# Optimization experiments

Hardware: AMD Instinct MI355X
Metric: run time of the kernel (lower is better)

Reference implementation:

```python
import jax, jax.numpy as jnp
import numpy as np
import math

T = 120      # frame_num == audio_len == max_seq_len
D = 64       # hidden_layer_size
H = 2        # n_head
DH = D // H
DFF = 2 * D
DOUT = 31
PERIOD = 10
EPS = 1e-5
NEG = -1e9
SCALE = 1.0 / math.sqrt(DH)
SLOPES = (1.0 / 16.0, 1.0 / 256.0)  # ALiBi slopes for n_head=2


def _pe():
    # PeriodicPositionalEncoding: sinusoid over one period, tiled
    pos = jnp.arange(PERIOD, dtype=jnp.float32)[:, None]
    div = jnp.exp(jnp.arange(0, D, 2, dtype=jnp.float32) * (-math.log(10000.0) / D))
    s, c = jnp.sin(pos * div), jnp.cos(pos * div)
    pe = jnp.stack([s, c], axis=-1).reshape(PERIOD, D)  # interleave sin/cos
    return jnp.tile(pe, (T // PERIOD + 1, 1))[:T]


def _alibi_mask():
    # causal mask + ALiBi bias: alibi[i,j] = -slope * floor((i-j)/period) for j<=i
    slopes = jnp.array(SLOPES, dtype=jnp.float32)
    i = jnp.arange(T)[:, None]
    j = jnp.arange(T)[None, :]
    rel = ((i - j) // PERIOD).astype(jnp.float32)
    return jnp.where(j <= i, -slopes[:, None, None] * rel, NEG)  # [H,T,T]


def _ln(x, g, b):
    m = x.mean(-1, keepdims=True)
    v = ((x - m) ** 2).mean(-1, keepdims=True)
    return (x - m) / jnp.sqrt(v + EPS) * g + b


def setup_inputs() -> dict:
    key = jax.random.key(0)
    ks = iter(jax.random.split(key, 32))
    n = lambda shape, s=0.05: jax.random.normal(next(ks), shape, dtype=jnp.float32) * s
    inp = {
        'audio': jax.random.normal(next(ks), (1, T, 1024), dtype=jnp.float32),
        'W_audio': n((D, 1024)), 'b_audio': n((D,)),
        'obj_W': n((D, 5)),
        'Wq': n((D, D)), 'bq': n((D,)), 'Wk': n((D, D)), 'bk': n((D,)),
        'Wv': n((D, D)), 'bv': n((D,)), 'Wo': n((D, D)), 'bo': n((D,)),
        'Wv2': n((D, D)), 'bv2': n((D,)), 'Wo2': n((D, D)), 'bo2': n((D,)),
        'g1': jnp.ones((D,)), 'be1': jnp.zeros((D,)),
        'g2': jnp.ones((D,)), 'be2': jnp.zeros((D,)),
        'g3': jnp.ones((D,)), 'be3': jnp.zeros((D,)),
        'W1': n((DFF, D)), 'c1': n((DFF,)), 'W2': n((D, DFF)), 'c2': n((D,)),
        'Wr': n((DOUT, D)), 'br': n((DOUT,)), 'Wm': n((D, DOUT)), 'bm': n((D,)),
    }
    return inp


def _forward(audio, W_audio, b_audio, obj_W, Wq, bq, Wk, bk, Wv, bv, Wo, bo,
             Wv2, bv2, Wo2, bo2, g1, be1, g2, be2, g3, be3,
             W1, c1, W2, c2, Wr, br, Wm, bm):
    mem = audio[0] @ W_audio.T + b_audio          # [S,D], S == T
    style = obj_W[:, 0]                            # obj_vector @ [1,0,0,0,0]
    pe = _pe()
    mask = _alibi_mask()
    slopes = jnp.array(SLOPES, dtype=jnp.float32)
    jarr = jnp.arange(T)

    # enc_dec_mask leaves exactly one memory key per target row (anti-diagonal
    # from the end); the feedback row t at step t always attends memory[-1],
    # so its cross-attn output is just the projected value of the last frame.
    cross_last = (mem[-1] @ Wv2.T + bv2) @ Wo2.T + bo2  # [D]

    def step(emb, t):
        # decode only the last row (row t) of the growing sequence; 1-layer
        # post-norm decoder => row t depends only on input rows 0..t.
        x = emb + pe                                 # PPE over prefix
        xq = jnp.take(x, t, axis=0)                  # [D]
        q = (xq @ Wq.T + bq).reshape(H, DH)
        k = (x @ Wk.T + bk).reshape(T, H, DH)
        v = (x @ Wv.T + bv).reshape(T, H, DH)
        bias = jnp.where(jarr <= t,
                         -slopes[:, None] * ((t - jarr) // PERIOD).astype(jnp.float32),
                         NEG)                        # [H,T]
        sc = jnp.einsum('hd,shd->hs', q, k) * SCALE + bias
        a = jax.nn.softmax(sc, axis=-1)
        sa = jnp.einsum('hs,shd->hd', a, v).reshape(D) @ Wo.T + bo
        h1 = _ln(xq + sa, g1, be1)
        h2 = _ln(h1 + cross_last, g2, be2)
        h3 = _ln(h2 + jax.nn.relu(h2 @ W1.T + c1) @ W2.T + c2, g3, be3)
        new = (h3 @ Wr.T + br) @ Wm.T + bm + style   # vertice_map(vertice_map_r(.)) + style
        emb = jax.lax.dynamic_update_slice(emb, new[None, :], (t + 1, 0))
        return emb, None

    emb0 = jnp.zeros((T, D), audio.dtype).at[0].set(style)
    emb, _ = jax.lax.scan(step, emb0, jnp.arange(T - 1))

    # final full-length decode (last loop iteration of the torch module)
    x = emb + pe
    q = (x @ Wq.T + bq).reshape(T, H, DH)
    k = (x @ Wk.T + bk).reshape(T, H, DH)
    v = (x @ Wv.T + bv).reshape(T, H, DH)
    sc = jnp.einsum('thd,shd->hts', q, k) * SCALE + mask
    a = jax.nn.softmax(sc, axis=-1)
    sa = jnp.einsum('hts,shd->thd', a, v).reshape(T, D) @ Wo.T + bo
    h1 = _ln(x + sa, g1, be1)
    # at length T with S == T the enc_dec_mask aligns target row j <-> memory row j
    cross = (mem @ Wv2.T + bv2) @ Wo2.T + bo2
    h2 = _ln(h1 + cross, g2, be2)
    h3 = _ln(h2 + jax.nn.relu(h2 @ W1.T + c1) @ W2.T + c2, g3, be3)
    return (h3 @ Wr.T + br)[None]                    # [1,T,31]


def reference(audio, W_audio, b_audio, obj_W, Wq, bq, Wk, bk, Wv, bv, Wo, bo,
              Wv2, bv2, Wo2, bo2, g1, be1, g2, be2, g3, be3,
              W1, c1, W2, c2, Wr, br, Wm, bm):
    return _forward(audio, W_audio, b_audio, obj_W, Wq, bq, Wk, bk, Wv, bv, Wo, bo,
                    Wv2, bv2, Wo2, bo2, g1, be1, g2, be2, g3, be3,
                    W1, c1, W2, c2, Wr, br, Wm, bm)
```

## Files before the change

kernel.cpp:

```cpp
#include <hip/hip_runtime.h>

typedef unsigned short u16;
typedef unsigned int   u32;
typedef _Float16 f16;
typedef f16 h2 __attribute__((ext_vector_type(2)));
typedef f16 h4 __attribute__((ext_vector_type(4)));
typedef f16 h8 __attribute__((ext_vector_type(8)));

#define T_    120
#define D_    64
#define DFF_  128
#define DOUT_ 31
#define KROW_ 68
#define VROW_ 132

#if defined(__has_builtin)
#if __has_builtin(__builtin_amdgcn_fdot2)
#define DOT2(a,b,c) __builtin_amdgcn_fdot2((a),(b),(c),false)
#endif
#endif
#ifndef DOT2
#define DOT2(a,b,c) ((float)(a).x*(float)(b).x + ((float)(a).y*(float)(b).y + (c)))
#endif
#define SHV(x,i,j) __builtin_shufflevector((x),(x),(i),(j))

__device__ __forceinline__ h2 pk(float a, float b){
#if defined(__has_builtin) && __has_builtin(__builtin_amdgcn_cvt_pkrtz)
  return __builtin_bit_cast(h2, __builtin_amdgcn_cvt_pkrtz(a, b));
#else
  h2 r; r.x = (f16)a; r.y = (f16)b; return r;
#endif
}

__device__ __forceinline__ float b2f(u16 u){ return __uint_as_float(((u32)u) << 16); }
__device__ __forceinline__ float2 bp2(u32 u){
  float2 r; r.x = __uint_as_float(u << 16); r.y = __uint_as_float(u & 0xffff0000u); return r;
}
__device__ __forceinline__ u16 f2bu(float f){
  u32 u = __float_as_uint(f);
  u32 r = u + 0x7fffu + ((u >> 16) & 1u);
  return (u16)(r >> 16);
}
#define WSYNC() do{ __asm__ __volatile__("" ::: "memory"); __builtin_amdgcn_wave_barrier(); }while(0)

__device__ __forceinline__ float dpp_sum(float x){
  int t;
  t = __builtin_amdgcn_update_dpp(0, __float_as_int(x), 0x111, 0xf, 0xf, true); x += __int_as_float(t);
  t = __builtin_amdgcn_update_dpp(0, __float_as_int(x), 0x112, 0xf, 0xf, true); x += __int_as_float(t);
  t = __builtin_amdgcn_update_dpp(0, __float_as_int(x), 0x114, 0xf, 0xf, true); x += __int_as_float(t);
  t = __builtin_amdgcn_update_dpp(0, __float_as_int(x), 0x118, 0xf, 0xf, true); x += __int_as_float(t);
  t = __builtin_amdgcn_update_dpp(0, __float_as_int(x), 0x142, 0xf, 0xf, true); x += __int_as_float(t);
  t = __builtin_amdgcn_update_dpp(0, __float_as_int(x), 0x143, 0xf, 0xf, true); x += __int_as_float(t);
  return __int_as_float(__builtin_amdgcn_readlane(__float_as_int(x), 63));
}
__device__ __forceinline__ float dpp_max_pos(float x){
  int t;
  t = __builtin_amdgcn_update_dpp(0, __float_as_int(x), 0x111, 0xf, 0xf, true); x = fmaxf(x, __int_as_float(t));
  t = __builtin_amdgcn_update_dpp(0, __float_as_int(x), 0x112, 0xf, 0xf, true); x = fmaxf(x, __int_as_float(t));
  t = __builtin_amdgcn_update_dpp(0, __float_as_int(x), 0x114, 0xf, 0xf, true); x = fmaxf(x, __int_as_float(t));
  t = __builtin_amdgcn_update_dpp(0, __float_as_int(x), 0x118, 0xf, 0xf, true); x = fmaxf(x, __int_as_float(t));
  t = __builtin_amdgcn_update_dpp(0, __float_as_int(x), 0x142, 0xf, 0xf, true); x = fmaxf(x, __int_as_float(t));
  t = __builtin_amdgcn_update_dpp(0, __float_as_int(x), 0x143, 0xf, 0xf, true); x = fmaxf(x, __int_as_float(t));
  return __int_as_float(__builtin_amdgcn_readlane(__float_as_int(x), 63));
}
__device__ __forceinline__ float pe_val(int row, int i){
  const float coef = -0.28782313662425574f;
  int p = row % 10;
  float dv  = __expf((float)(i >> 1) * coef);
  float ang = (float)p * dv;
  return (i & 1) ? __cosf(ang) : __sinf(ang);
}
__device__ __forceinline__ void loadrow32(h2* dst, const float* row){
  #pragma unroll
  for (int r = 0; r < 16; ++r){
    float4 f = ((const float4*)row)[r];
    dst[2*r]   = pk(f.x, f.y);
    dst[2*r+1] = pk(f.z, f.w);
  }
}
__device__ __forceinline__ void loadrow64(h2* dst, const float* row){
  #pragma unroll
  for (int r = 0; r < 32; ++r){
    float4 f = ((const float4*)row)[r];
    dst[2*r]   = pk(f.x, f.y);
    dst[2*r+1] = pk(f.z, f.w);
  }
}

__global__ __launch_bounds__(256) void k_prep(const float* __restrict__ Wv, const float* __restrict__ Wo,
                                              const float* __restrict__ W1, const float* __restrict__ W2,
                                              const float* __restrict__ Wr,
                                              u16* __restrict__ wvb, u16* __restrict__ wob,
                                              u16* __restrict__ w1b, u16* __restrict__ w2b,
                                              u16* __restrict__ wrb){
  int i0 = blockIdx.x*256 + threadIdx.x, stride = gridDim.x*256;
  for (int i = i0; i < 4096; i += stride){ wvb[i] = f2bu(Wv[i]); wob[i] = f2bu(Wo[i]); }
  for (int i = i0; i < 8192; i += stride){ w1b[i] = f2bu(W1[i]); w2b[i] = f2bu(W2[i]); }
  for (int i = i0; i < 1984; i += stride){ wrb[i] = f2bu(Wr[i]); }
}

__global__ __launch_bounds__(256) void k_mem(const float* __restrict__ audio,
                                             const float* __restrict__ Wa,
                                             const float* __restrict__ ba,
                                             float* __restrict__ mem){
  __shared__ float ash[1024];
  const int t = blockIdx.x, tid = threadIdx.x;
  for (int i = tid; i < 1024; i += 256) ash[i] = audio[t*1024 + i];
  __syncthreads();
  const int w = tid >> 6, lane = tid & 63;
  for (int d = w*16; d < w*16 + 16; ++d){
    const float4* row = (const float4*)(Wa + d*1024);
    float acc = 0.f;
    #pragma unroll
    for (int m = 0; m < 4; ++m){
      float4 wp = row[lane + 64*m];
      int j = 4*(lane + 64*m);
      acc += wp.x*ash[j] + wp.y*ash[j+1] + wp.z*ash[j+2] + wp.w*ash[j+3];
    }
    acc = dpp_sum(acc);
    if (lane == 0) mem[t*64 + d] = acc + ba[d];
  }
}

__global__ __launch_bounds__(64) void k_cross(const float* __restrict__ mem,
                                              const float* __restrict__ Wv2, const float* __restrict__ bv2,
                                              const float* __restrict__ Wo2, const float* __restrict__ bo2,
                                              float* __restrict__ cross){
  __shared__ float msh[64], tsh[64];
  const int t = blockIdx.x, i = threadIdx.x;
  msh[i] = mem[t*64 + i];
  __syncthreads();
  const float4* r1 = (const float4*)(Wv2 + i*64);
  float a = bv2[i];
  #pragma unroll
  for (int j = 0; j < 16; ++j){ float4 w = r1[j]; a += w.x*msh[4*j] + w.y*msh[4*j+1] + w.z*msh[4*j+2] + w.w*msh[4*j+3]; }
  tsh[i] = a;
  __syncthreads();
  const float4* r2 = (const float4*)(Wo2 + i*64);
  float c = bo2[i];
  #pragma unroll
  for (int j = 0; j < 16; ++j){ float4 w = r2[j]; c += w.x*tsh[4*j] + w.y*tsh[4*j+1] + w.z*tsh[4*j+2] + w.w*tsh[4*j+3]; }
  cross[t*64 + i] = c;
}

__global__ __launch_bounds__(128, 1) void k_scan(
    const float* __restrict__ objW,
    const float* __restrict__ Wq, const float* __restrict__ bq,
    const float* __restrict__ Wk, const float* __restrict__ bk,
    const float* __restrict__ Wv, const float* __restrict__ bv,
    const float* __restrict__ Wo, const float* __restrict__ bo,
    const float* __restrict__ g1, const float* __restrict__ be1,
    const float* __restrict__ g2, const float* __restrict__ be2,
    const float* __restrict__ g3, const float* __restrict__ be3,
    const float* __restrict__ W1, const float* __restrict__ c1,
    const float* __restrict__ W2, const float* __restrict__ c2,
    const float* __restrict__ Wr, const float* __restrict__ br,
    const float* __restrict__ Wm, const float* __restrict__ bm,
    const float* __restrict__ cross,
    float* __restrict__ xw, float* __restrict__ Kw, float* __restrict__ Vw)
{
  __shared__ __align__(16) f16 KcS[128*KROW_];
  __shared__ __align__(16) f16 VcS[D_*VROW_];
  __shared__ __align__(16) f16 sch[256];
  __shared__ __align__(16) f16 xh[64], qh[64], ath[64], h2h[64], h3h[64], rsh[32];
  __shared__ __align__(16) f16 fsh[128];
  __shared__ float at_p[64];
  __shared__ float pe_tab[640];

  const int tid = threadIdx.x;
  const int i = tid & 63;
  const bool w0 = tid < 64;

  h2 WA[32];
  h2 WB[32];
  h2 WOr[32], W1r[32], WRr[32], WMr[16];
  h2 W2r[64];
  float biasA=0.f, biasB=0.f, bo_r=0.f, c1r=0.f, c2_r=0.f, br_r=0.f, bmst=0.f, cls_r=0.f;
  float g1r=0.f,b1r=0.f,g2r=0.f,b2r=0.f,g3r=0.f,b3r=0.f, xr=0.f;

  if (w0){
    loadrow32(WA,  Wq + i*64);
    loadrow32(WB,  Wv + i*64);
    loadrow32(WOr, Wo + i*64);
    loadrow32(W1r, W1 + i*64);
    loadrow64(W2r, W2 + i*128);
    loadrow32(WRr, Wr + (i < 31 ? i : 30)*64);
    { const float* row = Wm + i*31;
      #pragma unroll
      for (int r = 0; r < 15; ++r) WMr[r] = pk(row[2*r], row[2*r+1]);
      WMr[15] = pk(row[30], 0.f); }
    biasA = bq[i]; biasB = bv[i]; bo_r = bo[i]; c1r = c1[i]; c2_r = c2[i];
    br_r = (i < 31) ? br[i] : 0.f;
    float st = objW[i*5];
    bmst = bm[i] + st;
    cls_r = cross[119*64 + i];
    g1r=g1[i]; b1r=be1[i]; g2r=g2[i]; b2r=be2[i]; g3r=g3[i]; b3r=be3[i];
    xr = st + pe_val(0, i);
    xh[i] = (f16)xr;
    xw[i] = xr;
  } else {
    loadrow32(WA, Wk + i*64);
    loadrow32(WB, W1 + (64+i)*64);
    biasA = bk[i]; c1r = c1[64+i];
  }
  { u32* kcw = (u32*)KcS; for (int idx = tid; idx < 128*KROW_/2; idx += 128) kcw[idx] = 0; }
  { u32* vcw = (u32*)VcS; for (int idx = tid; idx < D_*VROW_/2;  idx += 128) vcw[idx] = 0; }
  for (int idx = tid; idx < 640; idx += 128) pe_tab[idx] = pe_val(idx >> 6, idx & 63);
  if (tid < 32) rsh[tid] = (f16)0.f;
  __syncthreads();

  int pp = 1;
  for (int t = 0; t < T_-1; ++t){
    float atp0 = 0.f;
    {
      const h8* xv = (const h8*)xh;
      float a0=biasA, a1=0.f, a2=0.f, a3=0.f;
      #pragma unroll
      for (int r = 0; r < 8; ++r){
        h8 x = xv[r];
        a0 = DOT2(WA[4*r+0], SHV(x,0,1), a0);
        a1 = DOT2(WA[4*r+1], SHV(x,2,3), a1);
        a2 = DOT2(WA[4*r+2], SHV(x,4,5), a2);
        a3 = DOT2(WA[4*r+3], SHV(x,6,7), a3);
      }
      float accA = (a0+a1)+(a2+a3);
      if (w0){
        float b0=biasB, b1=0.f, b2=0.f, b3=0.f;
        #pragma unroll
        for (int r = 0; r < 8; ++r){
          h8 x = xv[r];
          b0 = DOT2(WB[4*r+0], SHV(x,0,1), b0);
          b1 = DOT2(WB[4*r+1], SHV(x,2,3), b1);
          b2 = DOT2(WB[4*r+2], SHV(x,4,5), b2);
          b3 = DOT2(WB[4*r+3], SHV(x,6,7), b3);
        }
        float accB = (b0+b1)+(b2+b3);
        qh[i] = (f16)accA;
        VcS[i*VROW_ + t] = (f16)accB;
        Vw[t*64 + i] = accB;
      } else {
        KcS[t*KROW_ + i] = (f16)accA;
        Kw[t*64 + i] = accA;
      }
    }
    __syncthreads();
    {
      const int h = tid >> 6, j = i;
      const h8* qv = (const h8*)(qh + h*32);
      const h4* k0 = (const h4*)(KcS + j*KROW_ + h*32);
      const h4* k1 = (const h4*)(KcS + (j+64)*KROW_ + h*32);
      float d0a=0.f,d0b=0.f,d1a=0.f,d1b=0.f;
      #pragma unroll
      for (int r = 0; r < 4; ++r){
        h8 q = qv[r];
        h4 ka = k0[2*r], kb = k0[2*r+1], kc = k1[2*r], kd = k1[2*r+1];
        d0a = DOT2(SHV(ka,0,1), SHV(q,0,1), d0a);
        d0b = DOT2(SHV(ka,2,3), SHV(q,2,3), d0b);
        d0a = DOT2(SHV(kb,0,1), SHV(q,4,5), d0a);
        d0b = DOT2(SHV(kb,2,3), SHV(q,6,7), d0b);
        d1a = DOT2(SHV(kc,0,1), SHV(q,0,1), d1a);
        d1b = DOT2(SHV(kc,2,3), SHV(q,2,3), d1b);
        d1a = DOT2(SHV(kd,0,1), SHV(q,4,5), d1a);
        d1b = DOT2(SHV(kd,2,3), SHV(q,6,7), d1b);
      }
      float d0 = d0a + d0b, d1 = d1a + d1b;
      const float slope = h ? 0.00390625f : 0.0625f;
      int r0 = (t - j) / 10, r1 = (t - j - 64) / 10;
      float s0 = (j      <= t) ? d0*0.17677669529663687f - slope*(float)r0 : -1e30f;
      float s1 = (j + 64 <= t) ? d1*0.17677669529663687f - slope*(float)r1 : -1e30f;
      float m = dpp_max_pos(fmaxf(s0, s1) + 16384.f) - 16384.f;
      float e0 = (j      <= t) ? __expf(s0 - m) : 0.f;
      float e1 = (j + 64 <= t) ? __expf(s1 - m) : 0.f;
      float inv = 1.f / dpp_sum(e0 + e1);
      sch[h*128 + j]      = (f16)(e0*inv);
      sch[h*128 + j + 64] = (f16)(e1*inv);
    }
    __syncthreads();
    {
      const int hd = i >> 5;
      const h8* av = (const h8*)(sch + hd*128) + (w0 ? 0 : 8);
      const h4* vv = (const h4*)(VcS + i*VROW_) + (w0 ? 0 : 16);
      float p0=0.f,p1=0.f,p2=0.f,p3=0.f;
      #pragma unroll
      for (int r = 0; r < 8; ++r){
        h8 a = av[r];
        h4 va = vv[2*r], vb = vv[2*r+1];
        p0 = DOT2(SHV(va,0,1), SHV(a,0,1), p0);
        p1 = DOT2(SHV(va,2,3), SHV(a,2,3), p1);
        p2 = DOT2(SHV(vb,0,1), SHV(a,4,5), p2);
        p3 = DOT2(SHV(vb,2,3), SHV(a,6,7), p3);
      }
      float p = (p0+p1)+(p2+p3);
      if (!w0) at_p[i] = p; else atp0 = p;
    }
    __syncthreads();
    if (w0){
      float atv = atp0 + at_p[i];
      ath[i] = (f16)atv;
      WSYNC();
      const h8* av = (const h8*)ath;
      float a0=bo_r, a1=0.f, a2=0.f, a3=0.f;
      #pragma unroll
      for (int r = 0; r < 8; ++r){
        h8 x = av[r];
        a0 = DOT2(WOr[4*r+0], SHV(x,0,1), a0);
        a1 = DOT2(WOr[4*r+1], SHV(x,2,3), a1);
        a2 = DOT2(WOr[4*r+2], SHV(x,4,5), a2);
        a3 = DOT2(WOr[4*r+3], SHV(x,6,7), a3);
      }
      float y = xr + (a0+a1)+(a2+a3);
      float s = dpp_sum(y), s2 = dpp_sum(y*y);
      float m = s*(1.f/64.f), var = fmaxf(s2*(1.f/64.f) - m*m, 0.f);
      float h1 = (y - m)*rsqrtf(var + 1e-5f)*g1r + b1r;
      float z = h1 + cls_r;
      float sz = dpp_sum(z), sz2 = dpp_sum(z*z);
      float mz = sz*(1.f/64.f), vz = fmaxf(sz2*(1.f/64.f) - mz*mz, 0.f);
      float h2v = (z - mz)*rsqrtf(vz + 1e-5f)*g2r + b2r;
      h2h[i] = (f16)h2v;
      at_p[i] = h2v;
    }
    __syncthreads();
    {
      const h8* hv = (const h8*)h2h;
      float a0=c1r, a1=0.f, a2=0.f, a3=0.f;
      if (w0){
        #pragma unroll
        for (int r = 0; r < 8; ++r){
          h8 x = hv[r];
          a0 = DOT2(W1r[4*r+0], SHV(x,0,1), a0);
          a1 = DOT2(W1r[4*r+1], SHV(x,2,3), a1);
          a2 = DOT2(W1r[4*r+2], SHV(x,4,5), a2);
          a3 = DOT2(W1r[4*r+3], SHV(x,6,7), a3);
        }
      } else {
        #pragma unroll
        for (int r = 0; r < 8; ++r){
          h8 x = hv[r];
          a0 = DOT2(WB[4*r+0], SHV(x,0,1), a0);
          a1 = DOT2(WB[4*r+1], SHV(x,2,3), a1);
          a2 = DOT2(WB[4*r+2], SHV(x,4,5), a2);
          a3 = DOT2(WB[4*r+3], SHV(x,6,7), a3);
        }
      }
      fsh[tid] = (f16)fmaxf((a0+a1)+(a2+a3), 0.f);
    }
    __syncthreads();
    if (w0){
      const h8* fv = (const h8*)fsh;
      float a0=c2_r, a1=0.f, a2=0.f, a3=0.f;
      #pragma unroll
      for (int r = 0; r < 16; ++r){
        h8 x = fv[r];
        a0 = DOT2(W2r[4*r+0], SHV(x,0,1), a0);
        a1 = DOT2(W2r[4*r+1], SHV(x,2,3), a1);
        a2 = DOT2(W2r[4*r+2], SHV(x,4,5), a2);
        a3 = DOT2(W2r[4*r+3], SHV(x,6,7), a3);
      }
      float y = at_p[i] + (a0+a1)+(a2+a3);
      float s = dpp_sum(y), s2 = dpp_sum(y*y);
      float m = s*(1.f/64.f), var = fmaxf(s2*(1.f/64.f) - m*m, 0.f);
      float h3v = (y - m)*rsqrtf(var + 1e-5f)*g3r + b3r;
      h3h[i] = (f16)h3v;
      WSYNC();
      const h8* h3v8 = (const h8*)h3h;
      float r0=br_r, r1=0.f, r2=0.f, r3=0.f;
      #pragma unroll
      for (int r = 0; r < 8; ++r){
        h8 x = h3v8[r];
        r0 = DOT2(WRr[4*r+0], SHV(x,0,1), r0);
        r1 = DOT2(WRr[4*r+1], SHV(x,2,3), r1);
        r2 = DOT2(WRr[4*r+2], SHV(x,4,5), r2);
        r3 = DOT2(WRr[4*r+3], SHV(x,6,7), r3);
      }
      if (i < 31) rsh[i] = (f16)((r0+r1)+(r2+r3));
      WSYNC();
      const h8* rv = (const h8*)rsh;
      float m0=bmst, m1=0.f, m2=0.f, m3=0.f;
      #pragma unroll
      for (int r = 0; r < 4; ++r){
        h8 x = rv[r];
        m0 = DOT2(WMr[4*r+0], SHV(x,0,1), m0);
        m1 = DOT2(WMr[4*r+1], SHV(x,2,3), m1);
        m2 = DOT2(WMr[4*r+2], SHV(x,4,5), m2);
        m3 = DOT2(WMr[4*r+3], SHV(x,6,7), m3);
      }
      float xn = (m0+m1)+(m2+m3) + pe_tab[pp*64 + i];
      xr = xn;
      xh[i] = (f16)xn;
      xw[(t+1)*64 + i] = xn;
    }
    __syncthreads();
    pp = (pp == 9) ? 0 : pp + 1;
  }
  {
    const h8* xv = (const h8*)xh;
    if (w0){
      float b0=biasB, b1=0.f, b2=0.f, b3=0.f;
      #pragma unroll
      for (int r = 0; r < 8; ++r){
        h8 x = xv[r];
        b0 = DOT2(WB[4*r+0], SHV(x,0,1), b0);
        b1 = DOT2(WB[4*r+1], SHV(x,2,3), b1);
        b2 = DOT2(WB[4*r+2], SHV(x,4,5), b2);
        b3 = DOT2(WB[4*r+3], SHV(x,6,7), b3);
      }
      Vw[119*64 + i] = (b0+b1)+(b2+b3);
    } else {
      float a0=biasA, a1=0.f, a2=0.f, a3=0.f;
      #pragma unroll
      for (int r = 0; r < 8; ++r){
        h8 x = xv[r];
        a0 = DOT2(WA[4*r+0], SHV(x,0,1), a0);
        a1 = DOT2(WA[4*r+1], SHV(x,2,3), a1);
        a2 = DOT2(WA[4*r+2], SHV(x,4,5), a2);
        a3 = DOT2(WA[4*r+3], SHV(x,6,7), a3);
      }
      Kw[119*64 + i] = (a0+a1)+(a2+a3);
    }
  }
}

__global__ __launch_bounds__(128) void k_final(
    const float* __restrict__ Wq, const float* __restrict__ bq, const float* __restrict__ bo,
    const float* __restrict__ g1, const float* __restrict__ be1,
    const float* __restrict__ g2, const float* __restrict__ be2,
    const float* __restrict__ g3, const float* __restrict__ be3,
    const float* __restrict__ c1, const float* __restrict__ c2, const float* __restrict__ br,
    const u16* __restrict__ wo_b, const u16* __restrict__ w1_b,
    const u16* __restrict__ w2_b, const u16* __restrict__ wr_b,
    const float* __restrict__ cross, const float* __restrict__ xw,
    const float* __restrict__ Kw, const float* __restrict__ Vw,
    float* __restrict__ out)
{
  __shared__ float xs[64], qs[64], at[64], h2s[64], h3s[64], fs[128], sc[256];
  const int irow = blockIdx.x, tid = threadIdx.x;
  if (tid < 64) xs[tid] = xw[irow*64 + tid];
  __syncthreads();
  if (tid < 64){
    const float4* wr_ = (const float4*)(Wq + tid*64);
    float acc = bq[tid];
    #pragma unroll
    for (int j = 0; j < 16; ++j){ float4 w = wr_[j]; acc += w.x*xs[4*j] + w.y*xs[4*j+1] + w.z*xs[4*j+2] + w.w*xs[4*j+3]; }
    qs[tid] = acc;
  }
  __syncthreads();
  {
    const int h = tid >> 6, j = tid & 63;
    const float* qh_ = qs + h*32;
    float d0 = 0.f, d1 = 0.f;
    const float4* k0 = (const float4*)(Kw + j*64 + h*32);
    #pragma unroll
    for (int w = 0; w < 8; ++w){ float4 p = k0[w]; d0 += p.x*qh_[4*w] + p.y*qh_[4*w+1] + p.z*qh_[4*w+2] + p.w*qh_[4*w+3]; }
    if (j < 56){
      const float4* k1 = (const float4*)(Kw + (j+64)*64 + h*32);
      #pragma unroll
      for (int w = 0; w < 8; ++w){ float4 p = k1[w]; d1 += p.x*qh_[4*w] + p.y*qh_[4*w+1] + p.z*qh_[4*w+2] + p.w*qh_[4*w+3]; }
    }
    const float slope = h ? 0.00390625f : 0.0625f;
    float s0 = (j      <= irow) ? d0*0.17677669529663687f - slope*(float)((irow-j)/10)    : -1e30f;
    float s1 = (j + 64 <= irow) ? d1*0.17677669529663687f - slope*(float)((irow-j-64)/10) : -1e30f;
    float m = dpp_max_pos(fmaxf(s0, s1) + 16384.f) - 16384.f;
    float e0 = (j      <= irow) ? __expf(s0 - m) : 0.f;
    float e1 = (j + 64 <= irow) ? __expf(s1 - m) : 0.f;
    float inv = 1.f / dpp_sum(e0 + e1);
    sc[h*128 + j]      = e0*inv;
    sc[h*128 + j + 64] = e1*inv;
  }
  __syncthreads();
  if (tid < 64){
    const float* a = sc + (tid >> 5)*128;
    float a0=0.f,a1=0.f,a2=0.f,a3=0.f;
    #pragma unroll
    for (int jj = 0; jj < 30; ++jj){
      a0 += a[4*jj]   * Vw[(4*jj)*64   + tid];
      a1 += a[4*jj+1] * Vw[(4*jj+1)*64 + tid];
      a2 += a[4*jj+2] * Vw[(4*jj+2)*64 + tid];
      a3 += a[4*jj+3] * Vw[(4*jj+3)*64 + tid];
    }
    at[tid] = (a0+a1)+(a2+a3);
  }
  __syncthreads();
  if (tid < 64){
    const u32* orow = (const u32*)(wo_b + tid*64);
    float acc = bo[tid];
    #pragma unroll
    for (int w = 0; w < 32; ++w){ float2 p = bp2(orow[w]); acc += p.x*at[2*w] + p.y*at[2*w+1]; }
    float y = xs[tid] + acc;
    float s = dpp_sum(y), s2 = dpp_sum(y*y);
    float m = s*(1.f/64.f), var = fmaxf(s2*(1.f/64.f) - m*m, 0.f);
    float h1 = (y - m)*rsqrtf(var + 1e-5f)*g1[tid] + be1[tid];
    float z = h1 + cross[irow*64 + tid];
    float sz = dpp_sum(z), sz2 = dpp_sum(z*z);
    float mz = sz*(1.f/64.f), vz = fmaxf(sz2*(1.f/64.f) - mz*mz, 0.f);
    h2s[tid] = (z - mz)*rsqrtf(vz + 1e-5f)*g2[tid] + be2[tid];
  }
  __syncthreads();
  {
    const u32* w1r = (const u32*)(w1_b + tid*64);
    float acc = c1[tid];
    #pragma unroll
    for (int w = 0; w < 32; ++w){ float2 p = bp2(w1r[w]); acc += p.x*h2s[2*w] + p.y*h2s[2*w+1]; }
    fs[tid] = fmaxf(acc, 0.f);
  }
  __syncthreads();
  if (tid < 64){
    const u32* w2r = (const u32*)(w2_b + tid*128);
    float acc = c2[tid];
    #pragma unroll
    for (int w = 0; w < 64; ++w){ float2 p = bp2(w2r[w]); acc += p.x*fs[2*w] + p.y*fs[2*w+1]; }
    float y = h2s[tid] + acc;
    float s = dpp_sum(y), s2 = dpp_sum(y*y);
    float m = s*(1.f/64.f), var = fmaxf(s2*(1.f/64.f) - m*m, 0.f);
    h3s[tid] = (y - m)*rsqrtf(var + 1e-5f)*g3[tid] + be3[tid];
  }
  __syncthreads();
  if (tid < DOUT_){
    const u32* rr = (const u32*)(wr_b + tid*64);
    float acc = br[tid];
    #pragma unroll
    for (int w = 0; w < 32; ++w){ float2 p = bp2(rr[w]); acc += p.x*h3s[2*w] + p.y*h3s[2*w+1]; }
    out[irow*DOUT_ + tid] = acc;
  }
}

extern "C" void kernel_launch(void* const* d_in, const int* in_sizes, int n_in,
                              void* d_out, int out_size, void* d_ws, size_t ws_size,
                              hipStream_t stream){
  const float* audio=(const float*)d_in[0];
  const float* Wa   =(const float*)d_in[1];
  const float* ba   =(const float*)d_in[2];
  const float* objW =(const float*)d_in[3];
  const float* Wq   =(const float*)d_in[4];
  const float* bq   =(const float*)d_in[5];
  const float* Wk   =(const float*)d_in[6];
  const float* bk   =(const float*)d_in[7];
  const float* Wv   =(const float*)d_in[8];
  const float* bv   =(const float*)d_in[9];
  const float* Wo   =(const float*)d_in[10];
  const float* bo   =(const float*)d_in[11];
  const float* Wv2  =(const float*)d_in[12];
  const float* bv2  =(const float*)d_in[13];
  const float* Wo2  =(const float*)d_in[14];
  const float* bo2  =(const float*)d_in[15];
  const float* g1   =(const float*)d_in[16];
  const float* be1  =(const float*)d_in[17];
  const float* g2   =(const float*)d_in[18];
  const float* be2  =(const float*)d_in[19];
  const float* g3   =(const float*)d_in[20];
  const float* be3  =(const float*)d_in[21];
  const float* W1   =(const float*)d_in[22];
  const float* c1   =(const float*)d_in[23];
  const float* W2   =(const float*)d_in[24];
  const float* c2   =(const float*)d_in[25];
  const float* Wr   =(const float*)d_in[26];
  const float* br   =(const float*)d_in[27];
  const float* Wm   =(const float*)d_in[28];
  const float* bm   =(const float*)d_in[29];

  float* ws    = (float*)d_ws;
  float* mem   = ws;
  float* cross = ws + 7680;
  float* xw    = ws + 15360;
  float* Kw    = ws + 23040;
  float* Vw    = ws + 30720;
  u16* bb   = (u16*)(ws + 38400);
  u16* wv_b = bb;
  u16* wo_b = bb + 4096;
  u16* w1_b = bb + 8192;
  u16* w2_b = bb + 16384;
  u16* wr_b = bb + 24576;
  float* out = (float*)d_out;

  k_prep <<<dim3(32),  dim3(256), 0, stream>>>(Wv, Wo, W1, W2, Wr, wv_b, wo_b, w1_b, w2_b, wr_b);
  k_mem  <<<dim3(120), dim3(256), 0, stream>>>(audio, Wa, ba, mem);
  k_cross<<<dim3(120), dim3(64),  0, stream>>>(mem, Wv2, bv2, Wo2, bo2, cross);
  k_scan <<<dim3(1),   dim3(128), 0, stream>>>(objW, Wq, bq, Wk, bk, Wv, bv, Wo, bo,
                                               g1, be1, g2, be2, g3, be3,
                                               W1, c1, W2, c2, Wr, br, Wm, bm,
                                               cross, xw, Kw, Vw);
  k_final<<<dim3(120), dim3(128), 0, stream>>>(Wq, bq, bo, g1, be1, g2, be2, g3, be3,
                                               c1, c2, br, wo_b, w1_b, w2_b, wr_b,
                                               cross, xw, Kw, Vw, out);
}
```

Before: 440.6 us.

## Fold Wm·Wr into one matrix, rebalance scan work across waves, fuse prep kernels

Precomputes Ms = Wm·Wr and bMv = Wm·br + bm, so the sequential scan step does one 64x64 matvec instead of two chained ones (64→31→64). The FFN second layer and the output/feedback path move to the second wave, which spreads register-held weights evenly across both waves and shortens the first wave's critical path. It also merges the prep, memory and cross kernels into one launch. K, V and x are kept in shared memory and written once as fp16 at the end, instead of fp32 global stores every step. The fused product and the fp16 storage change rounding slightly compared with the reference.

```diff
diff --git a/kernel.cpp b/kernel.cpp
--- a/kernel.cpp
+++ b/kernel.cpp
@@ -9,7 +9,6 @@
 
 #define T_    120
 #define D_    64
-#define DFF_  128
 #define DOUT_ 31
 #define KROW_ 68
 #define VROW_ 132
@@ -31,7 +30,6 @@
   h2 r; r.x = (f16)a; r.y = (f16)b; return r;
 #endif
 }
-
 __device__ __forceinline__ float b2f(u16 u){ return __uint_as_float(((u32)u) << 16); }
 __device__ __forceinline__ float2 bp2(u32 u){
   float2 r; r.x = __uint_as_float(u << 16); r.y = __uint_as_float(u & 0xffff0000u); return r;
@@ -40,6 +38,9 @@
   u32 u = __float_as_uint(f);
   u32 r = u + 0x7fffu + ((u >> 16) & 1u);
   return (u16)(r >> 16);
+}
+__device__ __forceinline__ u16 f2h16(float x){
+  f16 v = (f16)x; u16 r; __builtin_memcpy(&r, &v, 2); return r;
 }
 #define WSYNC() do{ __asm__ __volatile__("" ::: "memory"); __builtin_amdgcn_wave_barrier(); }while(0)
 
@@ -78,34 +79,42 @@
     dst[2*r+1] = pk(f.z, f.w);
   }
 }
-__device__ __forceinline__ void loadrow64(h2* dst, const float* row){
-  #pragma unroll
-  for (int r = 0; r < 32; ++r){
-    float4 f = ((const float4*)row)[r];
-    dst[2*r]   = pk(f.x, f.y);
-    dst[2*r+1] = pk(f.z, f.w);
-  }
-}
-
-__global__ __launch_bounds__(256) void k_prep(const float* __restrict__ Wv, const float* __restrict__ Wo,
-                                              const float* __restrict__ W1, const float* __restrict__ W2,
-                                              const float* __restrict__ Wr,
-                                              u16* __restrict__ wvb, u16* __restrict__ wob,
-                                              u16* __restrict__ w1b, u16* __restrict__ w2b,
-                                              u16* __restrict__ wrb){
-  int i0 = blockIdx.x*256 + threadIdx.x, stride = gridDim.x*256;
-  for (int i = i0; i < 4096; i += stride){ wvb[i] = f2bu(Wv[i]); wob[i] = f2bu(Wo[i]); }
-  for (int i = i0; i < 8192; i += stride){ w1b[i] = f2bu(W1[i]); w2b[i] = f2bu(W2[i]); }
-  for (int i = i0; i < 1984; i += stride){ wrb[i] = f2bu(Wr[i]); }
-}
-
-__global__ __launch_bounds__(256) void k_mem(const float* __restrict__ audio,
-                                             const float* __restrict__ Wa,
-                                             const float* __restrict__ ba,
-                                             float* __restrict__ mem){
+
+__global__ __launch_bounds__(256) void k_pre(const float* __restrict__ audio,
+                                             const float* __restrict__ Wa, const float* __restrict__ ba,
+                                             const float* __restrict__ Wv2, const float* __restrict__ bv2,
+                                             const float* __restrict__ Wo2, const float* __restrict__ bo2,
+                                             const float* __restrict__ Wo, const float* __restrict__ W1,
+                                             const float* __restrict__ W2, const float* __restrict__ Wr,
+                                             const float* __restrict__ Wm, const float* __restrict__ br,
+                                             const float* __restrict__ bm,
+                                             float* __restrict__ cross, float* __restrict__ Ms,
+                                             float* __restrict__ bMv,
+                                             u16* __restrict__ wob, u16* __restrict__ w1b,
+                                             u16* __restrict__ w2b, u16* __restrict__ wrb){
+  const int b = blockIdx.x, tid = threadIdx.x;
+  if (b == 120){
+    for (int i = tid; i < 4096; i += 256) wob[i] = f2bu(Wo[i]);
+    for (int i = tid; i < 8192; i += 256){ w1b[i] = f2bu(W1[i]); w2b[i] = f2bu(W2[i]); }
+    for (int i = tid; i < 1984; i += 256) wrb[i] = f2bu(Wr[i]);
+    for (int idx = tid; idx < 4096; idx += 256){
+      int d = idx >> 6, e = idx & 63;
+      float acc = 0.f;
+      #pragma unroll
+      for (int j = 0; j < 31; ++j) acc += Wm[d*31 + j] * Wr[j*64 + e];
+      Ms[idx] = acc;
+    }
+    if (tid < 64){
+      float acc = bm[tid];
+      #pragma unroll
+      for (int j = 0; j < 31; ++j) acc += Wm[tid*31 + j] * br[j];
+      bMv[tid] = acc;
+    }
+    return;
+  }
   __shared__ float ash[1024];
-  const int t = blockIdx.x, tid = threadIdx.x;
-  for (int i = tid; i < 1024; i += 256) ash[i] = audio[t*1024 + i];
+  __shared__ float msh[64], tsh[64];
+  for (int i = tid; i < 1024; i += 256) ash[i] = audio[b*1024 + i];
   __syncthreads();
   const int w = tid >> 6, lane = tid & 63;
   for (int d = w*16; d < w*16 + 16; ++d){
@@ -118,29 +127,24 @@
       acc += wp.x*ash[j] + wp.y*ash[j+1] + wp.z*ash[j+2] + wp.w*ash[j+3];
     }
     acc = dpp_sum(acc);
-    if (lane == 0) mem[t*64 + d] = acc + ba[d];
-  }
-}
-
-__global__ __launch_bounds__(64) void k_cross(const float* __restrict__ mem,
-                                              const float* __restrict__ Wv2, const float* __restrict__ bv2,
-                                              const float* __restrict__ Wo2, const float* __restrict__ bo2,
-                                              float* __restrict__ cross){
-  __shared__ float msh[64], tsh[64];
-  const int t = blockIdx.x, i = threadIdx.x;
-  msh[i] = mem[t*64 + i];
-  __syncthreads();
-  const float4* r1 = (const float4*)(Wv2 + i*64);
-  float a = bv2[i];
-  #pragma unroll
-  for (int j = 0; j < 16; ++j){ float4 w = r1[j]; a += w.x*msh[4*j] + w.y*msh[4*j+1] + w.z*msh[4*j+2] + w.w*msh[4*j+3]; }
-  tsh[i] = a;
-  __syncthreads();
-  const float4* r2 = (const float4*)(Wo2 + i*64);
-  float c = bo2[i];
-  #pragma unroll
-  for (int j = 0; j < 16; ++j){ float4 w = r2[j]; c += w.x*tsh[4*j] + w.y*tsh[4*j+1] + w.z*tsh[4*j+2] + w.w*tsh[4*j+3]; }
-  cross[t*64 + i] = c;
+    if (lane == 0) msh[d] = acc + ba[d];
+  }
+  __syncthreads();
+  if (tid < 64){
+    const float4* r1 = (const float4*)(Wv2 + tid*64);
+    float a = bv2[tid];
+    #pragma unroll
+    for (int j = 0; j < 16; ++j){ float4 p = r1[j]; a += p.x*msh[4*j] + p.y*msh[4*j+1] + p.z*msh[4*j+2] + p.w*msh[4*j+3]; }
+    tsh[tid] = a;
+  }
+  __syncthreads();
+  if (tid < 64){
+    const float4* r2 = (const float4*)(Wo2 + tid*64);
+    float c = bo2[tid];
+    #pragma unroll
+    for (int j = 0; j < 16; ++j){ float4 p = r2[j]; c += p.x*tsh[4*j] + p.y*tsh[4*j+1] + p.z*tsh[4*j+2] + p.w*tsh[4*j+3]; }
+    cross[b*64 + tid] = c;
+  }
 }
 
 __global__ __launch_bounds__(128, 1) void k_scan(
@@ -154,93 +158,83 @@
     const float* __restrict__ g3, const float* __restrict__ be3,
     const float* __restrict__ W1, const float* __restrict__ c1,
     const float* __restrict__ W2, const float* __restrict__ c2,
-    const float* __restrict__ Wr, const float* __restrict__ br,
-    const float* __restrict__ Wm, const float* __restrict__ bm,
+    const float* __restrict__ Ms, const float* __restrict__ bMv,
     const float* __restrict__ cross,
-    float* __restrict__ xw, float* __restrict__ Kw, float* __restrict__ Vw)
+    u16* __restrict__ xw16, u16* __restrict__ Kw16, u16* __restrict__ Vw16)
 {
   __shared__ __align__(16) f16 KcS[128*KROW_];
   __shared__ __align__(16) f16 VcS[D_*VROW_];
+  __shared__ __align__(16) f16 xwS[T_*D_];
   __shared__ __align__(16) f16 sch[256];
-  __shared__ __align__(16) f16 xh[64], qh[64], ath[64], h2h[64], h3h[64], rsh[32];
+  __shared__ __align__(16) f16 xh[64], qh[64], ath[64], h2h[64], h3h[64];
   __shared__ __align__(16) f16 fsh[128];
-  __shared__ float at_p[64];
+  __shared__ float at_p1[64], h2f[64], xf[64];
   __shared__ float pe_tab[640];
 
   const int tid = threadIdx.x;
   const int i = tid & 63;
   const bool w0 = tid < 64;
 
-  h2 WA[32];
-  h2 WB[32];
-  h2 WOr[32], W1r[32], WRr[32], WMr[16];
-  h2 W2r[64];
-  float biasA=0.f, biasB=0.f, bo_r=0.f, c1r=0.f, c2_r=0.f, br_r=0.f, bmst=0.f, cls_r=0.f;
-  float g1r=0.f,b1r=0.f,g2r=0.f,b2r=0.f,g3r=0.f,b3r=0.f, xr=0.f;
+  h2 A[32], B[32], C[32], D[32], E[32];
+  float biasA=0.f, biasB=0.f, bo_r=0.f, c1r=0.f, c2_r=0.f, bmst=0.f, cls_r=0.f;
+  float g1r=0.f,b1r=0.f,g2r=0.f,b2r=0.f,g3r=0.f,b3r=0.f;
 
   if (w0){
-    loadrow32(WA,  Wq + i*64);
-    loadrow32(WB,  Wv + i*64);
-    loadrow32(WOr, Wo + i*64);
-    loadrow32(W1r, W1 + i*64);
-    loadrow64(W2r, W2 + i*128);
-    loadrow32(WRr, Wr + (i < 31 ? i : 30)*64);
-    { const float* row = Wm + i*31;
-      #pragma unroll
-      for (int r = 0; r < 15; ++r) WMr[r] = pk(row[2*r], row[2*r+1]);
-      WMr[15] = pk(row[30], 0.f); }
-    biasA = bq[i]; biasB = bv[i]; bo_r = bo[i]; c1r = c1[i]; c2_r = c2[i];
-    br_r = (i < 31) ? br[i] : 0.f;
+    loadrow32(A, Wq + i*64);
+    loadrow32(B, Wv + i*64);
+    loadrow32(C, Wo + i*64);
+    loadrow32(D, W1 + i*64);
+    biasA = bq[i]; biasB = bv[i]; bo_r = bo[i]; c1r = c1[i];
+    g1r = g1[i]; b1r = be1[i]; g2r = g2[i]; b2r = be2[i];
+    cls_r = cross[119*64 + i];
+  } else {
+    loadrow32(A, Wk + i*64);
+    loadrow32(B, W1 + (64+i)*64);
+    loadrow32(C, W2 + i*128);
+    loadrow32(D, W2 + i*128 + 64);
+    loadrow32(E, Ms + i*64);
+    biasA = bk[i]; c1r = c1[64+i]; c2_r = c2[i];
+    g3r = g3[i]; b3r = be3[i];
+    bmst = bMv[i] + objW[i*5];
+  }
+  { u32* p = (u32*)KcS; for (int idx = tid; idx < 128*KROW_/2; idx += 128) p[idx] = 0; }
+  { u32* p = (u32*)VcS; for (int idx = tid; idx < D_*VROW_/2;  idx += 128) p[idx] = 0; }
+  for (int idx = tid; idx < 640; idx += 128) pe_tab[idx] = pe_val(idx >> 6, idx & 63);
+  if (w0){
     float st = objW[i*5];
-    bmst = bm[i] + st;
-    cls_r = cross[119*64 + i];
-    g1r=g1[i]; b1r=be1[i]; g2r=g2[i]; b2r=be2[i]; g3r=g3[i]; b3r=be3[i];
-    xr = st + pe_val(0, i);
-    xh[i] = (f16)xr;
-    xw[i] = xr;
-  } else {
-    loadrow32(WA, Wk + i*64);
-    loadrow32(WB, W1 + (64+i)*64);
-    biasA = bk[i]; c1r = c1[64+i];
-  }
-  { u32* kcw = (u32*)KcS; for (int idx = tid; idx < 128*KROW_/2; idx += 128) kcw[idx] = 0; }
-  { u32* vcw = (u32*)VcS; for (int idx = tid; idx < D_*VROW_/2;  idx += 128) vcw[idx] = 0; }
-  for (int idx = tid; idx < 640; idx += 128) pe_tab[idx] = pe_val(idx >> 6, idx & 63);
-  if (tid < 32) rsh[tid] = (f16)0.f;
+    float x0 = st + pe_val(0, i);
+    xf[i] = x0; xh[i] = (f16)x0; xwS[i] = (f16)x0;
+  }
   __syncthreads();
 
   int pp = 1;
   for (int t = 0; t < T_-1; ++t){
-    float atp0 = 0.f;
     {
       const h8* xv = (const h8*)xh;
-      float a0=biasA, a1=0.f, a2=0.f, a3=0.f;
-      #pragma unroll
-      for (int r = 0; r < 8; ++r){
-        h8 x = xv[r];
-        a0 = DOT2(WA[4*r+0], SHV(x,0,1), a0);
-        a1 = DOT2(WA[4*r+1], SHV(x,2,3), a1);
-        a2 = DOT2(WA[4*r+2], SHV(x,4,5), a2);
-        a3 = DOT2(WA[4*r+3], SHV(x,6,7), a3);
-      }
-      float accA = (a0+a1)+(a2+a3);
       if (w0){
-        float b0=biasB, b1=0.f, b2=0.f, b3=0.f;
+        float q0=biasA,q1=0.f,q2=0.f,q3=0.f, v0=biasB,v1=0.f,v2=0.f,v3=0.f;
         #pragma unroll
         for (int r = 0; r < 8; ++r){
           h8 x = xv[r];
-          b0 = DOT2(WB[4*r+0], SHV(x,0,1), b0);
-          b1 = DOT2(WB[4*r+1], SHV(x,2,3), b1);
-          b2 = DOT2(WB[4*r+2], SHV(x,4,5), b2);
-          b3 = DOT2(WB[4*r+3], SHV(x,6,7), b3);
+          h2 xa=SHV(x,0,1), xb=SHV(x,2,3), xc=SHV(x,4,5), xd=SHV(x,6,7);
+          q0 = DOT2(A[4*r+0], xa, q0); q1 = DOT2(A[4*r+1], xb, q1);
+          q2 = DOT2(A[4*r+2], xc, q2); q3 = DOT2(A[4*r+3], xd, q3);
+          v0 = DOT2(B[4*r+0], xa, v0); v1 = DOT2(B[4*r+1], xb, v1);
+          v2 = DOT2(B[4*r+2], xc, v2); v3 = DOT2(B[4*r+3], xd, v3);
         }
-        float accB = (b0+b1)+(b2+b3);
-        qh[i] = (f16)accA;
-        VcS[i*VROW_ + t] = (f16)accB;
-        Vw[t*64 + i] = accB;
+        qh[i] = (f16)((q0+q1)+(q2+q3));
+        VcS[i*VROW_ + t] = (f16)((v0+v1)+(v2+v3));
       } else {
-        KcS[t*KROW_ + i] = (f16)accA;
-        Kw[t*64 + i] = accA;
+        float k0=biasA,k1=0.f,k2=0.f,k3=0.f;
+        #pragma unroll
+        for (int r = 0; r < 8; ++r){
+          h8 x = xv[r];
+          k0 = DOT2(A[4*r+0], SHV(x,0,1), k0);
+          k1 = DOT2(A[4*r+1], SHV(x,2,3), k1);
+          k2 = DOT2(A[4*r+2], SHV(x,4,5), k2);
+          k3 = DOT2(A[4*r+3], SHV(x,6,7), k3);
+        }
+        KcS[t*KROW_ + i] = (f16)((k0+k1)+(k2+k3));
       }
     }
     __syncthreads();
@@ -276,6 +270,7 @@
       sch[h*128 + j + 64] = (f16)(e1*inv);
     }
     __syncthreads();
+    float atp0 = 0.f;
     {
       const int hd = i >> 5;
       const h8* av = (const h8*)(sch + hd*128) + (w0 ? 0 : 8);
@@ -291,11 +286,11 @@
         p3 = DOT2(SHV(vb,2,3), SHV(a,6,7), p3);
       }
       float p = (p0+p1)+(p2+p3);
-      if (!w0) at_p[i] = p; else atp0 = p;
+      if (!w0) at_p1[i] = p; else atp0 = p;
     }
     __syncthreads();
     if (w0){
-      float atv = atp0 + at_p[i];
+      float atv = atp0 + at_p1[i];
       ath[i] = (f16)atv;
       WSYNC();
       const h8* av = (const h8*)ath;
@@ -303,12 +298,12 @@
       #pragma unroll
       for (int r = 0; r < 8; ++r){
         h8 x = av[r];
-        a0 = DOT2(WOr[4*r+0], SHV(x,0,1), a0);
-        a1 = DOT2(WOr[4*r+1], SHV(x,2,3), a1);
-        a2 = DOT2(WOr[4*r+2], SHV(x,4,5), a2);
-        a3 = DOT2(WOr[4*r+3], SHV(x,6,7), a3);
-      }
-      float y = xr + (a0+a1)+(a2+a3);
+        a0 = DOT2(C[4*r+0], SHV(x,0,1), a0);
+        a1 = DOT2(C[4*r+1], SHV(x,2,3), a1);
+        a2 = DOT2(C[4*r+2], SHV(x,4,5), a2);
+        a3 = DOT2(C[4*r+3], SHV(x,6,7), a3);
+      }
+      float y = xf[i] + (a0+a1)+(a2+a3);
       float s = dpp_sum(y), s2 = dpp_sum(y*y);
       float m = s*(1.f/64.f), var = fmaxf(s2*(1.f/64.f) - m*m, 0.f);
       float h1 = (y - m)*rsqrtf(var + 1e-5f)*g1r + b1r;
@@ -317,7 +312,7 @@
       float mz = sz*(1.f/64.f), vz = fmaxf(sz2*(1.f/64.f) - mz*mz, 0.f);
       float h2v = (z - mz)*rsqrtf(vz + 1e-5f)*g2r + b2r;
       h2h[i] = (f16)h2v;
-      at_p[i] = h2v;
+      h2f[i] = h2v;
     }
     __syncthreads();
     {
@@ -327,67 +322,63 @@
         #pragma unroll
         for (int r = 0; r < 8; ++r){
           h8 x = hv[r];
-          a0 = DOT2(W1r[4*r+0], SHV(x,0,1), a0);
-          a1 = DOT2(W1r[4*r+1], SHV(x,2,3), a1);
-          a2 = DOT2(W1r[4*r+2], SHV(x,4,5), a2);
-          a3 = DOT2(W1r[4*r+3], SHV(x,6,7), a3);
+          a0 = DOT2(D[4*r+0], SHV(x,0,1), a0);
+          a1 = DOT2(D[4*r+1], SHV(x,2,3), a1);
+          a2 = DOT2(D[4*r+2], SHV(x,4,5), a2);
+          a3 = DOT2(D[4*r+3], SHV(x,6,7), a3);
         }
       } else {
         #pragma unroll
         for (int r = 0; r < 8; ++r){
           h8 x = hv[r];
-          a0 = DOT2(WB[4*r+0], SHV(x,0,1), a0);
-          a1 = DOT2(WB[4*r+1], SHV(x,2,3), a1);
-          a2 = DOT2(WB[4*r+2], SHV(x,4,5), a2);
-          a3 = DOT2(WB[4*r+3], SHV(x,6,7), a3);
+          a0 = DOT2(B[4*r+0], SHV(x,0,1), a0);
+          a1 = DOT2(B[4*r+1], SHV(x,2,3), a1);
+          a2 = DOT2(B[4*r+2], SHV(x,4,5), a2);
+          a3 = DOT2(B[4*r+3], SHV(x,6,7), a3);
         }
       }
       fsh[tid] = (f16)fmaxf((a0+a1)+(a2+a3), 0.f);
     }
     __syncthreads();
-    if (w0){
+    if (!w0){
       const h8* fv = (const h8*)fsh;
       float a0=c2_r, a1=0.f, a2=0.f, a3=0.f;
       #pragma unroll
-      for (int r = 0; r < 16; ++r){
+      for (int r = 0; r < 8; ++r){
         h8 x = fv[r];
-        a0 = DOT2(W2r[4*r+0], SHV(x,0,1), a0);
-        a1 = DOT2(W2r[4*r+1], SHV(x,2,3), a1);
-        a2 = DOT2(W2r[4*r+2], SHV(x,4,5), a2);
-        a3 = DOT2(W2r[4*r+3], SHV(x,6,7), a3);
-      }
-      float y = at_p[i] + (a0+a1)+(a2+a3);
+        a0 = DOT2(C[4*r+0], SHV(x,0,1), a0);
+        a1 = DOT2(C[4*r+1], SHV(x,2,3), a1);
+        a2 = DOT2(C[4*r+2], SHV(x,4,5), a2);
+        a3 = DOT2(C[4*r+3], SHV(x,6,7), a3);
+      }
+      #pragma unroll
+      for (int r = 0; r < 8; ++r){
+        h8 x = fv[8+r];
+        a0 = DOT2(D[4*r+0], SHV(x,0,1), a0);
+        a1 = DOT2(D[4*r+1], SHV(x,2,3), a1);
+        a2 = DOT2(D[4*r+2], SHV(x,4,5), a2);
+        a3 = DOT2(D[4*r+3], SHV(x,6,7), a3);
+      }
+      float y = h2f[i] + (a0+a1)+(a2+a3);
       float s = dpp_sum(y), s2 = dpp_sum(y*y);
       float m = s*(1.f/64.f), var = fmaxf(s2*(1.f/64.f) - m*m, 0.f);
       float h3v = (y - m)*rsqrtf(var + 1e-5f)*g3r + b3r;
       h3h[i] = (f16)h3v;
       WSYNC();
-      const h8* h3v8 = (const h8*)h3h;
-      float r0=br_r, r1=0.f, r2=0.f, r3=0.f;
-      #pragma unroll
-      for (int r = 0; r < 8; ++r){
-        h8 x = h3v8[r];
-        r0 = DOT2(WRr[4*r+0], SHV(x,0,1), r0);
-        r1 = DOT2(WRr[4*r+1], SHV(x,2,3), r1);
-        r2 = DOT2(WRr[4*r+2], SHV(x,4,5), r2);
-        r3 = DOT2(WRr[4*r+3], SHV(x,6,7), r3);
-      }
-      if (i < 31) rsh[i] = (f16)((r0+r1)+(r2+r3));
-      WSYNC();
-      const h8* rv = (const h8*)rsh;
+      const h8* hv3 = (const h8*)h3h;
       float m0=bmst, m1=0.f, m2=0.f, m3=0.f;
       #pragma unroll
-      for (int r = 0; r < 4; ++r){
-        h8 x = rv[r];
-        m0 = DOT2(WMr[4*r+0], SHV(x,0,1), m0);
-        m1 = DOT2(WMr[4*r+1], SHV(x,2,3), m1);
-        m2 = DOT2(WMr[4*r+2], SHV(x,4,5), m2);
-        m3 = DOT2(WMr[4*r+3], SHV(x,6,7), m3);
+      for (int r = 0; r < 8; ++r){
+        h8 x = hv3[r];
+        m0 = DOT2(E[4*r+0], SHV(x,0,1), m0);
+        m1 = DOT2(E[4*r+1], SHV(x,2,3), m1);
+        m2 = DOT2(E[4*r+2], SHV(x,4,5), m2);
+        m3 = DOT2(E[4*r+3], SHV(x,6,7), m3);
       }
       float xn = (m0+m1)+(m2+m3) + pe_tab[pp*64 + i];
-      xr = xn;
+      xf[i] = xn;
       xh[i] = (f16)xn;
-      xw[(t+1)*64 + i] = xn;
+      xwS[(t+1)*64 + i] = (f16)xn;
     }
     __syncthreads();
     pp = (pp == 9) ? 0 : pp + 1;
@@ -395,28 +386,39 @@
   {
     const h8* xv = (const h8*)xh;
     if (w0){
-      float b0=biasB, b1=0.f, b2=0.f, b3=0.f;
+      float v0=biasB,v1=0.f,v2=0.f,v3=0.f;
       #pragma unroll
       for (int r = 0; r < 8; ++r){
         h8 x = xv[r];
-        b0 = DOT2(WB[4*r+0], SHV(x,0,1), b0);
-        b1 = DOT2(WB[4*r+1], SHV(x,2,3), b1);
-        b2 = DOT2(WB[4*r+2], SHV(x,4,5), b2);
-        b3 = DOT2(WB[4*r+3], SHV(x,6,7), b3);
-      }
-      Vw[119*64 + i] = (b0+b1)+(b2+b3);
+        v0 = DOT2(B[4*r+0], SHV(x,0,1), v0);
+        v1 = DOT2(B[4*r+1], SHV(x,2,3), v1);
+        v2 = DOT2(B[4*r+2], SHV(x,4,5), v2);
+        v3 = DOT2(B[4*r+3], SHV(x,6,7), v3);
+      }
+      Vw16[119*64 + i] = f2h16((v0+v1)+(v2+v3));
     } else {
-      float a0=biasA, a1=0.f, a2=0.f, a3=0.f;
+      float k0=biasA,k1=0.f,k2=0.f,k3=0.f;
       #pragma unroll
       for (int r = 0; r < 8; ++r){
         h8 x = xv[r];
-        a0 = DOT2(WA[4*r+0], SHV(x,0,1), a0);
-        a1 = DOT2(WA[4*r+1], SHV(x,2,3), a1);
-        a2 = DOT2(WA[4*r+2], SHV(x,4,5), a2);
-        a3 = DOT2(WA[4*r+3], SHV(x,6,7), a3);
-      }
-      Kw[119*64 + i] = (a0+a1)+(a2+a3);
-    }
+        k0 = DOT2(A[4*r+0], SHV(x,0,1), k0);
+        k1 = DOT2(A[4*r+1], SHV(x,2,3), k1);
+        k2 = DOT2(A[4*r+2], SHV(x,4,5), k2);
+        k3 = DOT2(A[4*r+3], SHV(x,6,7), k3);
+      }
+      Kw16[119*64 + i] = f2h16((k0+k1)+(k2+k3));
+    }
+  }
+  {
+    const u16* kc = (const u16*)KcS;
+    const u16* vc = (const u16*)VcS;
+    for (int idx = tid; idx < 119*64; idx += 128){
+      int t_ = idx >> 6, d = idx & 63;
+      Kw16[idx] = kc[t_*KROW_ + d];
+      Vw16[idx] = vc[d*VROW_ + t_];
+    }
+    const u32* xs32 = (const u32*)xwS;
+    for (int idx = tid; idx < T_*D_/2; idx += 128) ((u32*)xw16)[idx] = xs32[idx];
   }
 }
 
@@ -428,13 +430,16 @@
     const float* __restrict__ c1, const float* __restrict__ c2, const float* __restrict__ br,
     const u16* __restrict__ wo_b, const u16* __restrict__ w1_b,
     const u16* __restrict__ w2_b, const u16* __restrict__ wr_b,
-    const float* __restrict__ cross, const float* __restrict__ xw,
-    const float* __restrict__ Kw, const float* __restrict__ Vw,
+    const float* __restrict__ cross, const u16* __restrict__ xw16,
+    const u16* __restrict__ Kw16, const u16* __restrict__ Vw16,
     float* __restrict__ out)
 {
   __shared__ float xs[64], qs[64], at[64], h2s[64], h3s[64], fs[128], sc[256];
   const int irow = blockIdx.x, tid = threadIdx.x;
-  if (tid < 64) xs[tid] = xw[irow*64 + tid];
+  const f16* xp = (const f16*)xw16;
+  const f16* kp = (const f16*)Kw16;
+  const f16* vp = (const f16*)Vw16;
+  if (tid < 64) xs[tid] = (float)xp[irow*64 + tid];
   __syncthreads();
   if (tid < 64){
     const float4* wr_ = (const float4*)(Wq + tid*64);
@@ -448,13 +453,19 @@
     const int h = tid >> 6, j = tid & 63;
     const float* qh_ = qs + h*32;
     float d0 = 0.f, d1 = 0.f;
-    const float4* k0 = (const float4*)(Kw + j*64 + h*32);
-    #pragma unroll
-    for (int w = 0; w < 8; ++w){ float4 p = k0[w]; d0 += p.x*qh_[4*w] + p.y*qh_[4*w+1] + p.z*qh_[4*w+2] + p.w*qh_[4*w+3]; }
+    const h4* k0 = (const h4*)(kp + j*64 + h*32);
+    #pragma unroll
+    for (int w = 0; w < 8; ++w){
+      h4 p = k0[w];
+      d0 += (float)p.x*qh_[4*w] + (float)p.y*qh_[4*w+1] + (float)p.z*qh_[4*w+2] + (float)p.w*qh_[4*w+3];
+    }
     if (j < 56){
-      const float4* k1 = (const float4*)(Kw + (j+64)*64 + h*32);
-      #pragma unroll
-      for (int w = 0; w < 8; ++w){ float4 p = k1[w]; d1 += p.x*qh_[4*w] + p.y*qh_[4*w+1] + p.z*qh_[4*w+2] + p.w*qh_[4*w+3]; }
+      const h4* k1 = (const h4*)(kp + (j+64)*64 + h*32);
+      #pragma unroll
+      for (int w = 0; w < 8; ++w){
+        h4 p = k1[w];
+        d1 += (float)p.x*qh_[4*w] + (float)p.y*qh_[4*w+1] + (float)p.z*qh_[4*w+2] + (float)p.w*qh_[4*w+3];
+      }
     }
     const float slope = h ? 0.00390625f : 0.0625f;
     float s0 = (j      <= irow) ? d0*0.17677669529663687f - slope*(float)((irow-j)/10)    : -1e30f;
@@ -472,10 +483,10 @@
     float a0=0.f,a1=0.f,a2=0.f,a3=0.f;
     #pragma unroll
     for (int jj = 0; jj < 30; ++jj){
-      a0 += a[4*jj]   * Vw[(4*jj)*64   + tid];
-      a1 += a[4*jj+1] * Vw[(4*jj+1)*64 + tid];
-      a2 += a[4*jj+2] * Vw[(4*jj+2)*64 + tid];
-      a3 += a[4*jj+3] * Vw[(4*jj+3)*64 + tid];
+      a0 += a[4*jj]   * (float)vp[(4*jj)*64   + tid];
+      a1 += a[4*jj+1] * (float)vp[(4*jj+1)*64 + tid];
+      a2 += a[4*jj+2] * (float)vp[(4*jj+2)*64 + tid];
+      a3 += a[4*jj+3] * (float)vp[(4*jj+3)*64 + tid];
     }
     at[tid] = (a0+a1)+(a2+a3);
   }
@@ -558,27 +569,26 @@
   const float* bm   =(const float*)d_in[29];
 
   float* ws    = (float*)d_ws;
-  float* mem   = ws;
-  float* cross = ws + 7680;
-  float* xw    = ws + 15360;
-  float* Kw    = ws + 23040;
-  float* Vw    = ws + 30720;
-  u16* bb   = (u16*)(ws + 38400);
-  u16* wv_b = bb;
-  u16* wo_b = bb + 4096;
-  u16* w1_b = bb + 8192;
-  u16* w2_b = bb + 16384;
-  u16* wr_b = bb + 24576;
+  float* cross = ws;
+  float* Ms    = ws + 7680;
+  float* bMv   = ws + 11776;
+  u16* xw16 = (u16*)(ws + 11840);
+  u16* Kw16 = xw16 + 7680;
+  u16* Vw16 = Kw16 + 7680;
+  u16* wo_b = Vw16 + 7680;
+  u16* w1_b = wo_b + 4096;
+  u16* w2_b = w1_b + 8192;
+  u16* wr_b = w2_b + 8192;
   float* out = (float*)d_out;
 
-  k_prep <<<dim3(32),  dim3(256), 0, stream>>>(Wv, Wo, W1, W2, Wr, wv_b, wo_b, w1_b, w2_b, wr_b);
-  k_mem  <<<dim3(120), dim3(256), 0, stream>>>(audio, Wa, ba, mem);
-  k_cross<<<dim3(120), dim3(64),  0, stream>>>(mem, Wv2, bv2, Wo2, bo2, cross);
+  k_pre  <<<dim3(121), dim3(256), 0, stream>>>(audio, Wa, ba, Wv2, bv2, Wo2, bo2,
+                                               Wo, W1, W2, Wr, Wm, br, bm,
+                                               cross, Ms, bMv, wo_b, w1_b, w2_b, wr_b);
   k_scan <<<dim3(1),   dim3(128), 0, stream>>>(objW, Wq, bq, Wk, bk, Wv, bv, Wo, bo,
                                                g1, be1, g2, be2, g3, be3,
-                                               W1, c1, W2, c2, Wr, br, Wm, bm,
-                                               cross, xw, Kw, Vw);
+                                               W1, c1, W2, c2, Ms, bMv,
+                                               cross, xw16, Kw16, Vw16);
   k_final<<<dim3(120), dim3(128), 0, stream>>>(Wq, bq, bo, g1, be1, g2, be2, g3, be3,
                                                c1, c2, br, wo_b, w1_b, w2_b, wr_b,
-                                               cross, xw, Kw, Vw, out);
-}
+                                               cross, xw16, Kw16, Vw16, out);
+}
```

Measured after the change: 390.2 us. 1.13x faster.
